# Kernel tuning notes

Measured on AMD Instinct MI355X. Metric: run time of the kernel, lower is better.

The kernel has to match this reference:

```python
import jax, jax.numpy as jnp
import numpy as np

B, T, H = 512, 128, 512
ZS, ZT = 128, 64
N_STATIC_CONT = 16
STATIC_CAT_KS = (8, 5, 12)
N_TEMP_CONT = 24
N_IRR = 2  # irreversible temp-cat indices 1 and 3; non-irr heads have widths 6,10,4
GRU_IN = ZT + H + 1 + N_IRR  # 579
TAU = 1.0


def _gumbel_softmax(logits, u, tau=TAU):
    # soft gumbel-softmax; u ~ Uniform(0,1), gumbel = -log(-log(u))
    g = -jnp.log(-jnp.log(u + 1e-10) + 1e-10)
    return jax.nn.softmax((logits + g) / tau, axis=-1)


def _gru_cell(x, h, Wih, Whh, bih, bhh):
    # PyTorch GRU cell semantics (gates in r,z,n order)
    gi = x @ Wih + bih
    gh = h @ Whh + bhh
    ir, iz, inn = jnp.split(gi, 3, axis=-1)
    hr, hz, hn = jnp.split(gh, 3, axis=-1)
    r = jax.nn.sigmoid(ir + hr)
    z = jax.nn.sigmoid(iz + hz)
    n = jnp.tanh(inn + r * hn)
    return (1.0 - z) * n + z * h


def setup_inputs():
    key = jax.random.key(0)
    ks = iter(jax.random.split(key, 64))
    def nrm(shape, fan_in):
        return jax.random.normal(next(ks), shape, jnp.float32) / np.sqrt(fan_in).astype(np.float32)
    def unif(shape):
        return jax.random.uniform(next(ks), shape, jnp.float32, 1e-6, 1.0 - 1e-6)
    return {
        "z_static": jax.random.normal(next(ks), (B, ZS), jnp.float32),
        "z_temporal": jax.random.normal(next(ks), (B, T, ZT), jnp.float32),
        "lengths": jax.random.randint(next(ks), (B,), 1, T + 1),
        "Ws1": nrm((ZS, H), ZS), "bs1": jnp.zeros((H,), jnp.float32),
        "Ws2": nrm((H, H), H), "bs2": jnp.zeros((H,), jnp.float32),
        "W_sc": nrm((H, N_STATIC_CONT), H), "b_sc": jnp.zeros((N_STATIC_CONT,), jnp.float32),
        "W_cat0": nrm((H, 8), H), "b_cat0": jnp.zeros((8,), jnp.float32),
        "W_cat1": nrm((H, 5), H), "b_cat1": jnp.zeros((5,), jnp.float32),
        "W_cat2": nrm((H, 12), H), "b_cat2": jnp.zeros((12,), jnp.float32),
        "W_irr": nrm((N_IRR, H, 2), H), "b_irr": jnp.zeros((N_IRR, 2), jnp.float32),
        "Wih0": nrm((GRU_IN, 3 * H), GRU_IN), "Whh0": nrm((H, 3 * H), H),
        "bih0": jnp.zeros((3 * H,), jnp.float32), "bhh0": jnp.zeros((3 * H,), jnp.float32),
        "Wih1": nrm((H, 3 * H), H), "Whh1": nrm((H, 3 * H), H),
        "bih1": jnp.zeros((3 * H,), jnp.float32), "bhh1": jnp.zeros((3 * H,), jnp.float32),
        "W_tc": nrm((H, N_TEMP_CONT), H), "b_tc": jnp.zeros((N_TEMP_CONT,), jnp.float32),
        "W_tcat0": nrm((H, 6), H), "b_tcat0": jnp.zeros((6,), jnp.float32),
        "W_tcat2": nrm((H, 10), H), "b_tcat2": jnp.zeros((10,), jnp.float32),
        "W_tcat4": nrm((H, 4), H), "b_tcat4": jnp.zeros((4,), jnp.float32),
        "W_hz": nrm((N_IRR, H + 1), H + 1), "b_hz": jnp.zeros((N_IRR,), jnp.float32),
        "u_sc0": unif((B, 8)), "u_sc1": unif((B, 5)), "u_sc2": unif((B, 12)),
        "u_irr": unif((N_IRR, B, 2)),
        "u_t0": unif((T, B, 6)), "u_t2": unif((T, B, 10)), "u_t4": unif((T, B, 4)),
        "u_bern": unif((T, B, N_IRR)),
    }


def reference(z_static, z_temporal, lengths, Ws1, bs1, Ws2, bs2, W_sc, b_sc,
              W_cat0, b_cat0, W_cat1, b_cat1, W_cat2, b_cat2, W_irr, b_irr,
              Wih0, Whh0, bih0, bhh0, Wih1, Whh1, bih1, bhh1,
              W_tc, b_tc, W_tcat0, b_tcat0, W_tcat2, b_tcat2, W_tcat4, b_tcat4,
              W_hz, b_hz, u_sc0, u_sc1, u_sc2, u_irr, u_t0, u_t2, u_t4, u_bern):
    baseline = jax.nn.relu(jax.nn.relu(z_static @ Ws1 + bs1) @ Ws2 + bs2)  # [B,H]
    static_cont = jax.nn.sigmoid(baseline @ W_sc + b_sc)
    static_cat = jnp.concatenate([
        _gumbel_softmax(baseline @ W_cat0 + b_cat0, u_sc0),
        _gumbel_softmax(baseline @ W_cat1 + b_cat1, u_sc1),
        _gumbel_softmax(baseline @ W_cat2 + b_cat2, u_sc2)], axis=-1)
    # init irreversible states = P(class 1) of 2-way gumbel-softmax per head
    irr0 = jnp.stack([
        _gumbel_softmax(baseline @ W_irr[j] + b_irr[j], u_irr[j])[:, 1]
        for j in range(N_IRR)], axis=-1)  # [B, N_IRR]
    tgrid = jnp.linspace(0.0, 1.0, T)
    visit_mask = (jnp.arange(T)[None, :] < lengths[:, None]).astype(jnp.float32)[..., None]  # [B,T,1]

    def step(carry, xs):
        h, irr = carry
        zt, ts, g0, g2, g4, ub = xs
        ts_col = jnp.broadcast_to(ts.reshape(1, 1), (zt.shape[0], 1))
        x = jnp.concatenate([zt, baseline, ts_col, irr], axis=-1)  # [B, GRU_IN]
        h0 = _gru_cell(x, h[0], Wih0, Whh0, bih0, bhh0)
        h1 = _gru_cell(h0, h[1], Wih1, Whh1, bih1, bhh1)
        out = h1
        tc = jax.nn.sigmoid(out @ W_tc + b_tc)
        # hazard heads take [out, t]; bernoulli flip only where not yet flipped
        haz = jax.nn.sigmoid(jnp.concatenate([out, ts_col], axis=-1) @ W_hz.T + b_hz)  # [B,N_IRR]
        flip = (ub < haz * (1.0 - irr)).astype(jnp.float32)
        irr_new = jnp.minimum(irr + flip, 1.0)
        tcat = jnp.concatenate([
            _gumbel_softmax(out @ W_tcat0 + b_tcat0, g0),
            irr_new[:, 0:1],
            _gumbel_softmax(out @ W_tcat2 + b_tcat2, g2),
            irr_new[:, 1:2],
            _gumbel_softmax(out @ W_tcat4 + b_tcat4, g4)], axis=-1)  # [B,22]
        return (jnp.stack([h0, h1]), irr_new), (tc, tcat)

    h_init = jnp.zeros((2, B, H), jnp.float32)
    _, (tc_seq, tcat_seq) = jax.lax.scan(
        step, (h_init, irr0),
        (jnp.swapaxes(z_temporal, 0, 1), tgrid, u_t0, u_t2, u_t4, u_bern))
    temporal_cont = jnp.swapaxes(tc_seq, 0, 1) * visit_mask  # [B,T,24]
    temporal_cat = jnp.swapaxes(tcat_seq, 0, 1) * visit_mask  # [B,T,22]
    visit_times = jnp.broadcast_to(tgrid[None, :], (B, T))
    return (static_cont, static_cat, temporal_cont, temporal_cat, visit_mask, visit_times)
```

## Files before the change

kernel.cpp:

```cpp
#include <hip/hip_runtime.h>


#define OFF_HID    0u
#define OFF_BASE   262144u
#define OFF_WHH0P  524288u
#define OFF_WIH1P  1310720u
#define OFF_WHH1P  2097152u
#define OFF_WMIDP  2883584u
#define OFF_WTOPP  3670016u
#define OFF_WTS    3768320u
#define OFF_WIRR   3769856u
#define OFF_GI0S   3772928u
#define OFF_H0X    4559360u
#define OFF_H1X    4821504u
#define OFF_HWTC   5083648u
#define OFF_HWHZ   5095936u
#define OFF_HWT0   5097088u
#define OFF_HWT2   5100160u
#define OFF_HWT4   5105280u
#define OFF_IRR0   5107328u
#define OFF_CTR    5108352u
#define OFF_END    5108864u

#define OUT_SC   0u
#define OUT_SCAT 8192u
#define OUT_TC   20992u
#define OUT_TCAT 1593856u
#define OUT_VM   3035648u
#define OUT_VT   3101184u

#define AS 516
#define RS 97

__device__ __forceinline__ float sigm(float x) { return 1.0f / (1.0f + expf(-x)); }
__device__ __forceinline__ float gumb(float u) { return -logf(-logf(u + 1e-10f) + 1e-10f); }
__device__ __forceinline__ float dot4(float4 a, float4 b) {
  return fmaf(a.x, b.x, fmaf(a.y, b.y, fmaf(a.z, b.z, a.w * b.w)));
}
__device__ __forceinline__ void astore(float* p, float v) {
  __hip_atomic_store(p, v, __ATOMIC_RELAXED, __HIP_MEMORY_SCOPE_AGENT);
}

__global__ __launch_bounds__(256) void pack_kernel(
    const float* __restrict__ Wih0, const float* __restrict__ Whh0,
    const float* __restrict__ Wih1, const float* __restrict__ Whh1,
    const float* __restrict__ W_tc, const float* __restrict__ W_hz,
    const float* __restrict__ W_tcat0, const float* __restrict__ W_tcat2,
    const float* __restrict__ W_tcat4, float* __restrict__ ws) {
  int idx = blockIdx.x * 256 + threadIdx.x;
  if (idx < 3145728) {
    int m = idx / 786432, r = idx % 786432;
    int s = r / 49152, t = r % 49152;
    if (m < 3) {
      int k4 = t / 384, rem = t % 384;
      int j = rem >> 7, u = (rem >> 2) & 31, ki = rem & 3;
      int k = 4 * k4 + ki;
      int col = j * 512 + s * 32 + u;
      const float* M = (m == 0) ? Whh0 : (m == 1) ? Wih1 : Whh1;
      unsigned dst = (m == 0) ? OFF_WHH0P : (m == 1) ? OFF_WIH1P : OFF_WHH1P;
      ws[dst + (unsigned)r] = M[k * 1536 + col];
    } else {
      int c = t / 512, k = t % 512;
      int col = (c % 3) * 512 + s * 32 + c / 3;
      ws[OFF_WMIDP + (unsigned)r] = Wih0[(64 + k) * 1536 + col];
    }
    return;
  }
  idx -= 3145728;
  if (idx < 98304) {
    int s = idx / 6144, t = idx % 6144;
    int k4 = t / 384, rem = t % 384;
    int j = rem >> 7, u = (rem >> 2) & 31, ki = rem & 3;
    int k = 4 * k4 + ki;
    int col = j * 512 + s * 32 + u;
    ws[OFF_WTOPP + (unsigned)idx] = Wih0[k * 1536 + col];
    return;
  }
  idx -= 98304;
  if (idx < 1536) {
    int s = idx / 96, c = idx % 96;
    ws[OFF_WTS + (unsigned)idx] = Wih0[576 * 1536 + (c % 3) * 512 + s * 32 + (c / 3)];
    return;
  }
  idx -= 1536;
  if (idx < 3072) {
    int s = idx / 192, m = (idx % 192) / 96, c = idx % 96;
    ws[OFF_WIRR + (unsigned)idx] = Wih0[(577 + m) * 1536 + (c % 3) * 512 + s * 32 + (c / 3)];
    return;
  }
  idx -= 3072;
  if (idx < 12288) { int c = idx / 512, k = idx % 512; ws[OFF_HWTC + (unsigned)idx] = W_tc[k * 24 + c]; return; }
  idx -= 12288;
  if (idx < 1032) {
    int c = idx / 516, j = idx % 516;
    ws[OFF_HWHZ + (unsigned)idx] = (j < 513) ? W_hz[c * 513 + j] : 0.0f;
    return;
  }
  idx -= 1032;
  if (idx < 3072) { int c = idx / 512, k = idx % 512; ws[OFF_HWT0 + (unsigned)idx] = W_tcat0[k * 6 + c]; return; }
  idx -= 3072;
  if (idx < 5120) { int c = idx / 512, k = idx % 512; ws[OFF_HWT2 + (unsigned)idx] = W_tcat2[k * 10 + c]; return; }
  idx -= 5120;
  if (idx < 2048) { int c = idx / 512, k = idx % 512; ws[OFF_HWT4 + (unsigned)idx] = W_tcat4[k * 4 + c]; }
}

template <int K>
__global__ __launch_bounds__(256) void mlp_kernel(
    const float* __restrict__ X, const float* __restrict__ Wm,
    const float* __restrict__ bias, float* __restrict__ Y) {
  __shared__ float Xs[4][K];
  const int rt = blockIdx.x, tid = threadIdx.x;
  for (int i = tid; i < 4 * K; i += 256) Xs[i / K][i % K] = X[(rt * 4 + i / K) * K + (i % K)];
  __syncthreads();
  float acc[4][2] = {};
  const int c0 = tid, c1 = tid + 256;
  for (int k = 0; k < K; ++k) {
    float w0 = Wm[k * 512 + c0], w1 = Wm[k * 512 + c1];
#pragma unroll
    for (int r = 0; r < 4; ++r) {
      acc[r][0] = fmaf(Xs[r][k], w0, acc[r][0]);
      acc[r][1] = fmaf(Xs[r][k], w1, acc[r][1]);
    }
  }
#pragma unroll
  for (int r = 0; r < 4; ++r) {
    Y[(rt * 4 + r) * 512 + c0] = fmaxf(acc[r][0] + bias[c0], 0.0f);
    Y[(rt * 4 + r) * 512 + c1] = fmaxf(acc[r][1] + bias[c1], 0.0f);
  }
}

__global__ __launch_bounds__(256) void gi0_kernel(
    const float* __restrict__ baseline, const float* __restrict__ WmidP,
    const float* __restrict__ bih0, float* __restrict__ gi0s) {
  __shared__ float As[64][128];
  __shared__ float Bs[96][129];
  const int s = blockIdx.x >> 3, rt = blockIdx.x & 7;
  const int tid = threadIdx.x, cg = tid & 31, rg = tid >> 5;
  float acc[8][3] = {};
  for (int kc = 0; kc < 4; ++kc) {
    for (int i = tid; i < 2048; i += 256) {
      int r = i >> 5, k4 = (i & 31) << 2;
      *(float4*)&As[r][k4] = *(const float4*)&baseline[(rt * 64 + r) * 512 + kc * 128 + k4];
    }
    for (int i = tid; i < 3072; i += 256) {
      int c = i >> 5, k4 = (i & 31) << 2;
      float4 v = *(const float4*)&WmidP[((unsigned)s * 96 + c) * 512 + kc * 128 + k4];
      Bs[c][k4] = v.x; Bs[c][k4 + 1] = v.y; Bs[c][k4 + 2] = v.z; Bs[c][k4 + 3] = v.w;
    }
    __syncthreads();
    for (int kk = 0; kk < 128; ++kk) {
      float b0 = Bs[3 * cg + 0][kk], b1 = Bs[3 * cg + 1][kk], b2 = Bs[3 * cg + 2][kk];
#pragma unroll
      for (int r = 0; r < 8; ++r) {
        float a = As[rg * 8 + r][kk];
        acc[r][0] = fmaf(a, b0, acc[r][0]);
        acc[r][1] = fmaf(a, b1, acc[r][1]);
        acc[r][2] = fmaf(a, b2, acc[r][2]);
      }
    }
    __syncthreads();
  }
#pragma unroll
  for (int r = 0; r < 8; ++r)
#pragma unroll
    for (int j = 0; j < 3; ++j) {
      int c = 3 * cg + j;
      gi0s[((unsigned)s * 512 + rt * 64 + rg * 8 + r) * 96 + c] = acc[r][j] + bih0[j * 512 + s * 32 + cg];
    }
}

__device__ void gumbel_write(const float* logits, int w, const float* u, float* dst) {
  float e[12]; float mx = -1e30f;
#pragma unroll
  for (int i = 0; i < 12; ++i) if (i < w) { e[i] = logits[i] + gumb(u[i]); mx = fmaxf(mx, e[i]); }
  float sum = 0.0f;
#pragma unroll
  for (int i = 0; i < 12; ++i) if (i < w) { e[i] = expf(e[i] - mx); sum += e[i]; }
  float inv = 1.0f / sum;
#pragma unroll
  for (int i = 0; i < 12; ++i) if (i < w) dst[i] = e[i] * inv;
}

__global__ __launch_bounds__(64) void static_heads_kernel(
    const float* __restrict__ baseline,
    const float* __restrict__ W_sc, const float* __restrict__ b_sc,
    const float* __restrict__ W_cat0, const float* __restrict__ b_cat0,
    const float* __restrict__ W_cat1, const float* __restrict__ b_cat1,
    const float* __restrict__ W_cat2, const float* __restrict__ b_cat2,
    const float* __restrict__ W_irr, const float* __restrict__ b_irr,
    const float* __restrict__ u_sc0, const float* __restrict__ u_sc1,
    const float* __restrict__ u_sc2, const float* __restrict__ u_irr,
    float* __restrict__ out, float* __restrict__ irr0buf) {
  const int b = blockIdx.x, tid = threadIdx.x;
  __shared__ float br[512];
  __shared__ float dots[48];
  for (int i = tid; i < 512; i += 64) br[i] = baseline[b * 512 + i];
  __syncthreads();
  if (tid < 45) {
    float d = 0.0f;
    if (tid < 16) { for (int k = 0; k < 512; ++k) d = fmaf(br[k], W_sc[k * 16 + tid], d); d += b_sc[tid]; }
    else if (tid < 24) { int c = tid - 16; for (int k = 0; k < 512; ++k) d = fmaf(br[k], W_cat0[k * 8 + c], d); d += b_cat0[c]; }
    else if (tid < 29) { int c = tid - 24; for (int k = 0; k < 512; ++k) d = fmaf(br[k], W_cat1[k * 5 + c], d); d += b_cat1[c]; }
    else if (tid < 41) { int c = tid - 29; for (int k = 0; k < 512; ++k) d = fmaf(br[k], W_cat2[k * 12 + c], d); d += b_cat2[c]; }
    else { int i = tid - 41, j = i >> 1, cls = i & 1;
           for (int k = 0; k < 512; ++k) d = fmaf(br[k], W_irr[j * 1024 + k * 2 + cls], d);
           d += b_irr[j * 2 + cls]; }
    dots[tid] = d;
  }
  __syncthreads();
  if (tid < 16) out[OUT_SC + b * 16 + tid] = sigm(dots[tid]);
  else if (tid == 16) gumbel_write(&dots[16], 8,  u_sc0 + b * 8,  out + OUT_SCAT + b * 25 + 0);
  else if (tid == 17) gumbel_write(&dots[24], 5,  u_sc1 + b * 5,  out + OUT_SCAT + b * 25 + 8);
  else if (tid == 18) gumbel_write(&dots[29], 12, u_sc2 + b * 12, out + OUT_SCAT + b * 25 + 13);
  else if (tid == 19 || tid == 20) {
    int j = tid - 19;
    float e0 = dots[41 + 2 * j] + gumb(u_irr[j * 1024 + b * 2 + 0]);
    float e1 = dots[42 + 2 * j] + gumb(u_irr[j * 1024 + b * 2 + 1]);
    float mx = fmaxf(e0, e1);
    float x0 = expf(e0 - mx), x1 = expf(e1 - mx);
    irr0buf[b * 2 + j] = x1 / (x0 + x1);
  }
}

__global__ __launch_bounds__(1024, 4) void recurrence_kernel(
    float* ws, const float* __restrict__ z_temporal, const int* __restrict__ lengths,
    const float* __restrict__ bhh0, const float* __restrict__ bih1, const float* __restrict__ bhh1,
    const float* __restrict__ b_tc, const float* __restrict__ b_hz,
    const float* __restrict__ b_tcat0, const float* __restrict__ b_tcat2,
    const float* __restrict__ b_tcat4,
    const float* __restrict__ u_t0, const float* __restrict__ u_t2,
    const float* __restrict__ u_t4, const float* __restrict__ u_bern,
    float* __restrict__ out) {
  const int tid = threadIdx.x;
  const int s = blockIdx.x & 15;
  const int g = blockIdx.x >> 4;
  const int b0 = g * 32;
  const int lane = tid & 63, wv = tid >> 6;
  const int kh = wv >> 3;
  const int cq = (wv >> 1) & 3;
  const int rh = wv & 1;
  const int u8 = lane & 7;
  const int rg8 = lane >> 3;
  const int unit = 8 * cq + u8;
  const int jglob = s * 32 + unit;
  const int row0 = 16 * rh + rg8;
  const int hrow = tid >> 5, kp = tid & 31;

  __shared__ __align__(16) float A0[32 * AS];
  __shared__ __align__(16) float A1[32 * AS];
  __shared__ __align__(16) float Rbuf[2 * 32 * RS];
  __shared__ float irr_l[32][2];

  float* h0x = ws + OFF_H0X;
  float* h1x = ws + OFF_H1X;
  unsigned* ctr = ((unsigned*)(ws + OFF_CTR)) + g * 32;

  const float* WpA = ws + OFF_WHH0P + (unsigned)s * 49152;
  const float* WpI = ws + OFF_WIH1P + (unsigned)s * 49152;
  const float* WpH = ws + OFF_WHH1P + (unsigned)s * 49152;
  const float* WpT = ws + OFF_WTOPP + (unsigned)s * 6144;

  const int c0u = 3 * unit;
  const float* wtsp  = ws + OFF_WTS + s * 96;
  const float* wirrp = ws + OFF_WIRR + s * 192;
  const float* gi0p  = ws + OFF_GI0S + ((unsigned)s * 512 + b0) * 96;
  float wts0 = wtsp[c0u], wts1 = wtsp[c0u + 1], wts2 = wtsp[c0u + 2];
  float wi00 = wirrp[c0u], wi01 = wirrp[c0u + 1], wi02 = wirrp[c0u + 2];
  float wi10 = wirrp[96 + c0u], wi11 = wirrp[96 + c0u + 1], wi12 = wirrp[96 + c0u + 2];
  float g0s[2][3];
#pragma unroll
  for (int q = 0; q < 2; ++q)
#pragma unroll
    for (int j = 0; j < 3; ++j) g0s[q][j] = gi0p[(row0 + 8 * q) * 96 + c0u + j];
  float bh0r = bhh0[jglob], bh0z = bhh0[512 + jglob], bh0n = bhh0[1024 + jglob];
  float bi1r = bih1[jglob], bi1z = bih1[512 + jglob], bi1n = bih1[1024 + jglob];
  float bh1r = bhh1[jglob], bh1z = bhh1[512 + jglob], bh1n = bhh1[1024 + jglob];
  float bhz0 = b_hz[0], bhz1 = b_hz[1];

  for (int i = tid; i < 32 * AS; i += 1024) { A0[i] = 0.0f; A1[i] = 0.0f; }
  if (tid < 64) irr_l[tid >> 1][tid & 1] = ws[OFF_IRR0 + (b0 + (tid >> 1)) * 2 + (tid & 1)];
  __syncthreads();

  unsigned bart = 0;
  auto barrive = [&]() {
    __builtin_amdgcn_s_waitcnt(0);
    __syncthreads();
    bart += 16;
    if (tid == 0)
      __hip_atomic_fetch_add(ctr, 1u, __ATOMIC_RELEASE, __HIP_MEMORY_SCOPE_AGENT);
  };
  auto barwait = [&]() {
    if (tid == 0) {
      while (__hip_atomic_load(ctr, __ATOMIC_RELAXED, __HIP_MEMORY_SCOPE_AGENT) < bart)
        __builtin_amdgcn_s_sleep(1);
    }
    __syncthreads();
    __asm__ __volatile__("" ::: "memory");
  };

  float4 sv[4];
  auto stage_issue = [&](const float* src) {
#pragma unroll
    for (int j = 0; j < 4; ++j) {
      int slot = j * 1024 + tid;
      asm volatile("global_load_dwordx4 %0, %1, off sc1"
                   : "=v"(sv[j]) : "v"(src + (slot >> 7) * 512 + ((slot & 127) << 2)));
    }
  };
  auto stage_finish = [&](float* dstLDS) {
    asm volatile("s_waitcnt vmcnt(0)" ::: "memory");
#pragma unroll
    for (int j = 0; j < 4; ++j) {
      int slot = j * 1024 + tid;
      *(float4*)(dstLDS + (slot >> 7) * AS + ((slot & 127) << 2)) = sv[j];
    }
    __syncthreads();
  };

  auto gemmKS = [&](const float* A, const float* Bp, float (&acc)[2][3]) {
    const float* bp = Bp + (unsigned)(kh * 64) * 384 + (unsigned)unit * 4;
    const float* ap = A + (unsigned)row0 * AS + kh * 256;
#pragma unroll 4
    for (int k4 = 0; k4 < 64; ++k4) {
      const float* p = bp + (unsigned)k4 * 384;
      float4 w0 = *(const float4*)(p);
      float4 w1 = *(const float4*)(p + 128);
      float4 w2 = *(const float4*)(p + 256);
      float4 av[2];
#pragma unroll
      for (int q = 0; q < 2; ++q) av[q] = *(const float4*)(ap + q * (8 * AS) + k4 * 4);
      const float* w0a = (const float*)&w0;
      const float* w1a = (const float*)&w1;
      const float* w2a = (const float*)&w2;
#pragma unroll
      for (int q = 0; q < 2; ++q) {
        const float* aa = (const float*)&av[q];
#pragma unroll
        for (int i = 0; i < 4; ++i) {
          acc[q][0] = fmaf(aa[i], w0a[i], acc[q][0]);
          acc[q][1] = fmaf(aa[i], w1a[i], acc[q][1]);
          acc[q][2] = fmaf(aa[i], w2a[i], acc[q][2]);
        }
      }
    }
  };

  auto gemmZ = [&](int t, float (&acc)[2][3]) {
    const float* bp = WpT + (unsigned)(kh * 8) * 384 + (unsigned)unit * 4;
#pragma unroll 2
    for (int k4 = 0; k4 < 8; ++k4) {
      const float* p = bp + (unsigned)k4 * 384;
      float4 w0 = *(const float4*)(p);
      float4 w1 = *(const float4*)(p + 128);
      float4 w2 = *(const float4*)(p + 256);
      const float* w0a = (const float*)&w0;
      const float* w1a = (const float*)&w1;
      const float* w2a = (const float*)&w2;
#pragma unroll
      for (int q = 0; q < 2; ++q) {
        int row = b0 + row0 + 8 * q;
        float4 zv = *(const float4*)(z_temporal + ((unsigned)row * 128 + t) * 64 + kh * 32 + k4 * 4);
        const float* aa = (const float*)&zv;
#pragma unroll
        for (int i = 0; i < 4; ++i) {
          acc[q][0] = fmaf(aa[i], w0a[i], acc[q][0]);
          acc[q][1] = fmaf(aa[i], w1a[i], acc[q][1]);
          acc[q][2] = fmaf(aa[i], w2a[i], acc[q][2]);
        }
      }
    }
  };

  auto reduce2 = [&](float (&aX)[2][3], float (&aY)[2][3]) {
    if (kh == 1) {
#pragma unroll
      for (int q = 0; q < 2; ++q) {
        int row = row0 + 8 * q;
        float* p0 = Rbuf + row * RS + c0u;
        float* p1 = Rbuf + 32 * RS + row * RS + c0u;
        p0[0] = aX[q][0]; p0[1] = aX[q][1]; p0[2] = aX[q][2];
        p1[0] = aY[q][0]; p1[1] = aY[q][1]; p1[2] = aY[q][2];
      }
    }
    __syncthreads();
    if (kh == 0) {
#pragma unroll
      for (int q = 0; q < 2; ++q) {
        int row = row0 + 8 * q;
        const float* p0 = Rbuf + row * RS + c0u;
        const float* p1 = Rbuf + 32 * RS + row * RS + c0u;
        aX[q][0] += p0[0]; aX[q][1] += p0[1]; aX[q][2] += p0[2];
        aY[q][0] += p1[0]; aY[q][1] += p1[1]; aY[q][2] += p1[2];
      }
    }
  };

  auto do_heads = [&](int tp) {
    const float tsp = (float)tp * (1.0f / 127.0f);
    const float* Ar = A1 + hrow * AS;
    {
      const float* hz = ws + OFF_HWHZ;
      float d0 = 0.0f, d1 = 0.0f;
#pragma unroll
      for (int i = 0; i < 4; ++i) {
        int k = kp * 4 + 128 * i;
        float4 x = *(const float4*)(Ar + k);
        d0 += dot4(x, *(const float4*)(hz + k));
        d1 += dot4(x, *(const float4*)(hz + 516 + k));
      }
#pragma unroll
      for (int off = 1; off < 32; off <<= 1) { d0 += __shfl_xor(d0, off, 32); d1 += __shfl_xor(d1, off, 32); }
      if (kp == 0) {
        float h0v = sigm(d0 + tsp * hz[512] + bhz0);
        float h1v = sigm(d1 + tsp * hz[516 + 512] + bhz1);
        float i0 = irr_l[hrow][0], i1 = irr_l[hrow][1];
        const float* ub = u_bern + ((unsigned)tp * 512 + b0 + hrow) * 2;
        irr_l[hrow][0] = fminf(i0 + ((ub[0] < h0v * (1.0f - i0)) ? 1.0f : 0.0f), 1.0f);
        irr_l[hrow][1] = fminf(i1 + ((ub[1] < h1v * (1.0f - i1)) ? 1.0f : 0.0f), 1.0f);
      }
    }
    if (s < 12) {
      const float* wt = ws + OFF_HWTC + (unsigned)(2 * s) * 512;
      float d0 = 0.0f, d1 = 0.0f;
#pragma unroll
      for (int i = 0; i < 4; ++i) {
        int k = kp * 4 + 128 * i;
        float4 x = *(const float4*)(Ar + k);
        d0 += dot4(x, *(const float4*)(wt + k));
        d1 += dot4(x, *(const float4*)(wt + 512 + k));
      }
#pragma unroll
      for (int off = 1; off < 32; off <<= 1) { d0 += __shfl_xor(d0, off, 32); d1 += __shfl_xor(d1, off, 32); }
      if (kp == 0) {
        int brow = b0 + hrow;
        float msk = (tp < lengths[brow]) ? 1.0f : 0.0f;
        float* o = out + OUT_TC + ((unsigned)brow * 128 + tp) * 24 + 2 * s;
        o[0] = sigm(d0 + b_tc[2 * s]) * msk;
        o[1] = sigm(d1 + b_tc[2 * s + 1]) * msk;
      }
    } else if (s == 15) {
      if (kp == 0) {
        int brow = b0 + hrow;
        float msk = (tp < lengths[brow]) ? 1.0f : 0.0f;
        out[OUT_TCAT + ((unsigned)brow * 128 + tp) * 22 + 6]  = irr_l[hrow][0] * msk;
        out[OUT_TCAT + ((unsigned)brow * 128 + tp) * 22 + 17] = irr_l[hrow][1] * msk;
        out[OUT_VM + (unsigned)brow * 128 + tp] = msk;
        out[OUT_VT + (unsigned)brow * 128 + tp] = tsp;
      }
    } else {
      const int w = (s == 12) ? 6 : (s == 13) ? 10 : 4;
      const float* WT = ws + ((s == 12) ? OFF_HWT0 : (s == 13) ? OFF_HWT2 : OFF_HWT4);
      const float* bt = (s == 12) ? b_tcat0 : (s == 13) ? b_tcat2 : b_tcat4;
      const float* ut = (s == 12) ? u_t0 : (s == 13) ? u_t2 : u_t4;
      const int cbase = (s == 12) ? 0 : (s == 13) ? 7 : 18;
      float lg[10];
#pragma unroll
      for (int c = 0; c < 10; ++c) lg[c] = 0.0f;
#pragma unroll
      for (int i = 0; i < 4; ++i) {
        int k = kp * 4 + 128 * i;
        float4 x = *(const float4*)(Ar + k);
        for (int c = 0; c < w; ++c)
          lg[c] += dot4(x, *(const float4*)(WT + (unsigned)c * 512 + k));
      }
      for (int c = 0; c < w; ++c) {
#pragma unroll
        for (int off = 1; off < 32; off <<= 1) lg[c] += __shfl_xor(lg[c], off, 32);
      }
      if (kp == 0) {
        int brow = b0 + hrow;
        float msk = (tp < lengths[brow]) ? 1.0f : 0.0f;
        float e[10], mx = -1e30f;
        for (int c = 0; c < w; ++c) {
          float uu = ut[((unsigned)tp * 512 + brow) * (unsigned)w + c];
          e[c] = lg[c] + bt[c] + gumb(uu); mx = fmaxf(mx, e[c]);
        }
        float sum = 0.0f;
        for (int c = 0; c < w; ++c) { e[c] = expf(e[c] - mx); sum += e[c]; }
        float inv = 1.0f / sum;
        float* o = out + OUT_TCAT + ((unsigned)brow * 128 + tp) * 22 + cbase;
        for (int c = 0; c < w; ++c) o[c] = e[c] * inv * msk;
      }
    }
    __syncthreads();
  };

  float accH[2][3] = {};
  for (int t = 0; t < 128; ++t) {
    const float tsv = (float)t * (1.0f / 127.0f);

    float accI[2][3] = {};
    gemmZ(t, accI);

    if (t > 0) {
      stage_finish(A1);
      do_heads(t - 1);
    }

    reduce2(accH, accI);
    if (kh == 0) {
#pragma unroll
      for (int q = 0; q < 2; ++q) {
        int row = row0 + 8 * q;
        float i0 = irr_l[row][0], i1 = irr_l[row][1];
        float gir = accI[q][0] + g0s[q][0] + tsv * wts0 + i0 * wi00 + i1 * wi10;
        float giz = accI[q][1] + g0s[q][1] + tsv * wts1 + i0 * wi01 + i1 * wi11;
        float gin = accI[q][2] + g0s[q][2] + tsv * wts2 + i0 * wi02 + i1 * wi12;
        float rr = sigm(gir + accH[q][0] + bh0r);
        float zz = sigm(giz + accH[q][1] + bh0z);
        float nn = tanhf(gin + rr * (accH[q][2] + bh0n));
        float hp = A0[row * AS + jglob];
        astore(h0x + (unsigned)(b0 + row) * 512 + jglob, (1.0f - zz) * nn + zz * hp);
      }
    }

    barrive();
    float accH2[2][3] = {};
    gemmKS(A1, WpH, accH2);
    barwait();

    stage_issue(h0x + b0 * 512);
    stage_finish(A0);

    float accI2[2][3] = {};
    gemmKS(A0, WpI, accI2);
    reduce2(accH2, accI2);
    if (kh == 0) {
#pragma unroll
      for (int q = 0; q < 2; ++q) {
        int row = row0 + 8 * q;
        float rr = sigm(accI2[q][0] + bi1r + accH2[q][0] + bh1r);
        float zz = sigm(accI2[q][1] + bi1z + accH2[q][1] + bh1z);
        float nn = tanhf(accI2[q][2] + bi1n + rr * (accH2[q][2] + bh1n));
        float hp = A1[row * AS + jglob];
        astore(h1x + (unsigned)(b0 + row) * 512 + jglob, (1.0f - zz) * nn + zz * hp);
      }
    }

    barrive();
#pragma unroll
    for (int q = 0; q < 2; ++q) { accH[q][0] = accH[q][1] = accH[q][2] = 0.0f; }
    gemmKS(A0, WpA, accH);
    barwait();

    stage_issue(h1x + b0 * 512);
  }
  stage_finish(A1);
  do_heads(127);
}

extern "C" void kernel_launch(void* const* d_in, const int* in_sizes, int n_in,
                              void* d_out, int out_size, void* d_ws, size_t ws_size,
                              hipStream_t stream) {
  const float* z_static   = (const float*)d_in[0];
  const float* z_temporal = (const float*)d_in[1];
  const int*   lengths    = (const int*)d_in[2];
  const float* Ws1 = (const float*)d_in[3];
  const float* bs1 = (const float*)d_in[4];
  const float* Ws2 = (const float*)d_in[5];
  const float* bs2 = (const float*)d_in[6];
  const float* W_sc = (const float*)d_in[7];
  const float* b_sc = (const float*)d_in[8];
  const float* W_cat0 = (const float*)d_in[9];
  const float* b_cat0 = (const float*)d_in[10];
  const float* W_cat1 = (const float*)d_in[11];
  const float* b_cat1 = (const float*)d_in[12];
  const float* W_cat2 = (const float*)d_in[13];
  const float* b_cat2 = (const float*)d_in[14];
  const float* W_irr = (const float*)d_in[15];
  const float* b_irr = (const float*)d_in[16];
  const float* Wih0 = (const float*)d_in[17];
  const float* Whh0 = (const float*)d_in[18];
  const float* bih0 = (const float*)d_in[19];
  const float* bhh0 = (const float*)d_in[20];
  const float* Wih1 = (const float*)d_in[21];
  const float* Whh1 = (const float*)d_in[22];
  const float* bih1 = (const float*)d_in[23];
  const float* bhh1 = (const float*)d_in[24];
  const float* W_tc = (const float*)d_in[25];
  const float* b_tc = (const float*)d_in[26];
  const float* W_tcat0 = (const float*)d_in[27];
  const float* b_tcat0 = (const float*)d_in[28];
  const float* W_tcat2 = (const float*)d_in[29];
  const float* b_tcat2 = (const float*)d_in[30];
  const float* W_tcat4 = (const float*)d_in[31];
  const float* b_tcat4 = (const float*)d_in[32];
  const float* W_hz = (const float*)d_in[33];
  const float* b_hz = (const float*)d_in[34];
  const float* u_sc0 = (const float*)d_in[35];
  const float* u_sc1 = (const float*)d_in[36];
  const float* u_sc2 = (const float*)d_in[37];
  const float* u_irr = (const float*)d_in[38];
  const float* u_t0 = (const float*)d_in[39];
  const float* u_t2 = (const float*)d_in[40];
  const float* u_t4 = (const float*)d_in[41];
  const float* u_bern = (const float*)d_in[42];

  float* ws = (float*)d_ws;
  float* out = (float*)d_out;

  hipMemsetAsync((void*)(ws + OFF_CTR), 0, (size_t)(OFF_END - OFF_CTR) * sizeof(float), stream);

  pack_kernel<<<12783, 256, 0, stream>>>(Wih0, Whh0, Wih1, Whh1,
      W_tc, W_hz, W_tcat0, W_tcat2, W_tcat4, ws);
  mlp_kernel<128><<<128, 256, 0, stream>>>(z_static, Ws1, bs1, ws + OFF_HID);
  mlp_kernel<512><<<128, 256, 0, stream>>>(ws + OFF_HID, Ws2, bs2, ws + OFF_BASE);
  static_heads_kernel<<<512, 64, 0, stream>>>(ws + OFF_BASE, W_sc, b_sc,
      W_cat0, b_cat0, W_cat1, b_cat1, W_cat2, b_cat2, W_irr, b_irr,
      u_sc0, u_sc1, u_sc2, u_irr, out, ws + OFF_IRR0);
  gi0_kernel<<<128, 256, 0, stream>>>(ws + OFF_BASE, ws + OFF_WMIDP, bih0, ws + OFF_GI0S);
  recurrence_kernel<<<256, 1024, 0, stream>>>(ws, z_temporal, lengths,
      bhh0, bih1, bhh1, b_tc, b_hz, b_tcat0, b_tcat2, b_tcat4,
      u_t0, u_t2, u_t4, u_bern, out);
}
```

Before: 13.75 ms.

## Fuse Wih1 and Whh0 GEMMs over shared A0 with 4-way K-split register tiles

Interleaves the Wih1 and next-step Whh0 weight panels so a single pass over the freshly staged layer-0 hidden state computes both layer-1 input gates and the next layer-0 recurrent gates. The tiling changes from a 2-way K split with 2 rows x 1 unit per thread to a 4-way K split with 2 rows x 2 units per thread, reduced through shared memory in two stages. The z_temporal projection for the next step is moved into the barrier wait window, and the cell constants and biases are packed into one float4-readable table. The aim is fewer passes over A0, more register reuse per load, and hidden latency in the cross-block barrier, at the cost of extra __syncthreads in the reduction and higher register pressure.

```diff
diff --git a/kernel.cpp b/kernel.cpp
--- a/kernel.cpp
+++ b/kernel.cpp
@@ -3,24 +3,22 @@
 
 #define OFF_HID    0u
 #define OFF_BASE   262144u
-#define OFF_WHH0P  524288u
-#define OFF_WIH1P  1310720u
+#define OFF_WFUSE  524288u
 #define OFF_WHH1P  2097152u
 #define OFF_WMIDP  2883584u
 #define OFF_WTOPP  3670016u
-#define OFF_WTS    3768320u
-#define OFF_WIRR   3769856u
-#define OFF_GI0S   3772928u
-#define OFF_H0X    4559360u
-#define OFF_H1X    4821504u
-#define OFF_HWTC   5083648u
-#define OFF_HWHZ   5095936u
-#define OFF_HWT0   5097088u
-#define OFF_HWT2   5100160u
-#define OFF_HWT4   5105280u
-#define OFF_IRR0   5107328u
-#define OFF_CTR    5108352u
-#define OFF_END    5108864u
+#define OFF_CELLC  3768320u
+#define OFF_GI0S   3778560u
+#define OFF_H0X    4827136u
+#define OFF_H1X    5089280u
+#define OFF_HWTC   5351424u
+#define OFF_HWHZ   5363712u
+#define OFF_HWT0   5364752u
+#define OFF_HWT2   5367824u
+#define OFF_HWT4   5372944u
+#define OFF_IRR0   5374992u
+#define OFF_CTR    5376016u
+#define OFF_END    5376528u
 
 #define OUT_SC   0u
 #define OUT_SCAT 8192u
@@ -44,51 +42,72 @@
 __global__ __launch_bounds__(256) void pack_kernel(
     const float* __restrict__ Wih0, const float* __restrict__ Whh0,
     const float* __restrict__ Wih1, const float* __restrict__ Whh1,
+    const float* __restrict__ bhh0, const float* __restrict__ bih1,
+    const float* __restrict__ bhh1,
     const float* __restrict__ W_tc, const float* __restrict__ W_hz,
     const float* __restrict__ W_tcat0, const float* __restrict__ W_tcat2,
     const float* __restrict__ W_tcat4, float* __restrict__ ws) {
   int idx = blockIdx.x * 256 + threadIdx.x;
-  if (idx < 3145728) {
-    int m = idx / 786432, r = idx % 786432;
-    int s = r / 49152, t = r % 49152;
-    if (m < 3) {
-      int k4 = t / 384, rem = t % 384;
-      int j = rem >> 7, u = (rem >> 2) & 31, ki = rem & 3;
-      int k = 4 * k4 + ki;
-      int col = j * 512 + s * 32 + u;
-      const float* M = (m == 0) ? Whh0 : (m == 1) ? Wih1 : Whh1;
-      unsigned dst = (m == 0) ? OFF_WHH0P : (m == 1) ? OFF_WIH1P : OFF_WHH1P;
-      ws[dst + (unsigned)r] = M[k * 1536 + col];
-    } else {
-      int c = t / 512, k = t % 512;
-      int col = (c % 3) * 512 + s * 32 + c / 3;
-      ws[OFF_WMIDP + (unsigned)r] = Wih0[(64 + k) * 1536 + col];
-    }
+  if (idx < 1572864) {
+    int s = idx / 98304, t = idx % 98304;
+    int k2 = t / 384, rem = t % 384;
+    int panel = rem / 192, rem2 = rem % 192;
+    int gate = rem2 / 64, rem3 = rem2 % 64;
+    int pr = rem3 >> 2, q = rem3 & 3;
+    int pair = q >> 1, ki = q & 1;
+    int k = 2 * k2 + ki;
+    int col = gate * 512 + s * 32 + pair * 16 + pr;
+    ws[OFF_WFUSE + (unsigned)idx] = panel ? Whh0[k * 1536 + col] : Wih1[k * 1536 + col];
     return;
   }
-  idx -= 3145728;
+  idx -= 1572864;
+  if (idx < 786432) {
+    int s = idx / 49152, t = idx % 49152;
+    int k4 = t / 384, rem = t % 384;
+    int gate = rem / 128, rem2 = rem % 128;
+    int pair = rem2 / 64, rem3 = rem2 % 64;
+    int pr = rem3 >> 2, ki = rem3 & 3;
+    int k = 4 * k4 + ki;
+    int col = gate * 512 + s * 32 + pair * 16 + pr;
+    ws[OFF_WHH1P + (unsigned)idx] = Whh1[k * 1536 + col];
+    return;
+  }
+  idx -= 786432;
+  if (idx < 786432) {
+    int s = idx / 49152, t = idx % 49152;
+    int c = t / 512, k = t % 512;
+    int col = (c % 3) * 512 + s * 32 + c / 3;
+    ws[OFF_WMIDP + (unsigned)idx] = Wih0[(64 + k) * 1536 + col];
+    return;
+  }
+  idx -= 786432;
   if (idx < 98304) {
     int s = idx / 6144, t = idx % 6144;
     int k4 = t / 384, rem = t % 384;
-    int j = rem >> 7, u = (rem >> 2) & 31, ki = rem & 3;
+    int gate = rem / 128, rem2 = rem % 128;
+    int pair = rem2 / 64, rem3 = rem2 % 64;
+    int pr = rem3 >> 2, ki = rem3 & 3;
     int k = 4 * k4 + ki;
-    int col = j * 512 + s * 32 + u;
+    int col = gate * 512 + s * 32 + pair * 16 + pr;
     ws[OFF_WTOPP + (unsigned)idx] = Wih0[k * 1536 + col];
     return;
   }
   idx -= 98304;
-  if (idx < 1536) {
-    int s = idx / 96, c = idx % 96;
-    ws[OFF_WTS + (unsigned)idx] = Wih0[576 * 1536 + (c % 3) * 512 + s * 32 + (c / 3)];
+  if (idx < 10240) {
+    int s = idx / 640, rem = idx % 640;
+    int unit = rem / 20, q = rem % 20;
+    int base = s * 32 + unit;
+    float v = 0.0f;
+    if (q < 3)       v = Wih0[576 * 1536 + q * 512 + base];
+    else if (q < 6)  v = Wih0[577 * 1536 + (q - 3) * 512 + base];
+    else if (q < 9)  v = Wih0[578 * 1536 + (q - 6) * 512 + base];
+    else if (q < 12) v = bhh0[(q - 9) * 512 + base];
+    else if (q < 15) v = bih1[(q - 12) * 512 + base];
+    else if (q < 18) v = bhh1[(q - 15) * 512 + base];
+    ws[OFF_CELLC + (unsigned)idx] = v;
     return;
   }
-  idx -= 1536;
-  if (idx < 3072) {
-    int s = idx / 192, m = (idx % 192) / 96, c = idx % 96;
-    ws[OFF_WIRR + (unsigned)idx] = Wih0[(577 + m) * 1536 + (c % 3) * 512 + s * 32 + (c / 3)];
-    return;
-  }
-  idx -= 3072;
+  idx -= 10240;
   if (idx < 12288) { int c = idx / 512, k = idx % 512; ws[OFF_HWTC + (unsigned)idx] = W_tc[k * 24 + c]; return; }
   idx -= 12288;
   if (idx < 1032) {
@@ -164,8 +183,8 @@
   for (int r = 0; r < 8; ++r)
 #pragma unroll
     for (int j = 0; j < 3; ++j) {
-      int c = 3 * cg + j;
-      gi0s[((unsigned)s * 512 + rt * 64 + rg * 8 + r) * 96 + c] = acc[r][j] + bih0[j * 512 + s * 32 + cg];
+      gi0s[(((unsigned)s * 512 + rt * 64 + rg * 8 + r) * 32 + cg) * 4 + j] =
+          acc[r][j] + bih0[j * 512 + s * 32 + cg];
     }
 }
 
@@ -224,7 +243,6 @@
 
 __global__ __launch_bounds__(1024, 4) void recurrence_kernel(
     float* ws, const float* __restrict__ z_temporal, const int* __restrict__ lengths,
-    const float* __restrict__ bhh0, const float* __restrict__ bih1, const float* __restrict__ bhh1,
     const float* __restrict__ b_tc, const float* __restrict__ b_hz,
     const float* __restrict__ b_tcat0, const float* __restrict__ b_tcat2,
     const float* __restrict__ b_tcat4,
@@ -236,14 +254,11 @@
   const int g = blockIdx.x >> 4;
   const int b0 = g * 32;
   const int lane = tid & 63, wv = tid >> 6;
-  const int kh = wv >> 3;
-  const int cq = (wv >> 1) & 3;
-  const int rh = wv & 1;
-  const int u8 = lane & 7;
-  const int rg8 = lane >> 3;
-  const int unit = 8 * cq + u8;
-  const int jglob = s * 32 + unit;
-  const int row0 = 16 * rh + rg8;
+  const int kh = wv >> 2;
+  const int rv = wv & 3;
+  const int pr = lane & 15;
+  const int rs = lane >> 4;
+  const int r0 = rv * 8 + rs * 2;
   const int hrow = tid >> 5, kp = tid & 31;
 
   __shared__ __align__(16) float A0[32 * AS];
@@ -255,26 +270,11 @@
   float* h1x = ws + OFF_H1X;
   unsigned* ctr = ((unsigned*)(ws + OFF_CTR)) + g * 32;
 
-  const float* WpA = ws + OFF_WHH0P + (unsigned)s * 49152;
-  const float* WpI = ws + OFF_WIH1P + (unsigned)s * 49152;
+  const float* WpF = ws + OFF_WFUSE + (unsigned)s * 98304;
   const float* WpH = ws + OFF_WHH1P + (unsigned)s * 49152;
   const float* WpT = ws + OFF_WTOPP + (unsigned)s * 6144;
-
-  const int c0u = 3 * unit;
-  const float* wtsp  = ws + OFF_WTS + s * 96;
-  const float* wirrp = ws + OFF_WIRR + s * 192;
-  const float* gi0p  = ws + OFF_GI0S + ((unsigned)s * 512 + b0) * 96;
-  float wts0 = wtsp[c0u], wts1 = wtsp[c0u + 1], wts2 = wtsp[c0u + 2];
-  float wi00 = wirrp[c0u], wi01 = wirrp[c0u + 1], wi02 = wirrp[c0u + 2];
-  float wi10 = wirrp[96 + c0u], wi11 = wirrp[96 + c0u + 1], wi12 = wirrp[96 + c0u + 2];
-  float g0s[2][3];
-#pragma unroll
-  for (int q = 0; q < 2; ++q)
-#pragma unroll
-    for (int j = 0; j < 3; ++j) g0s[q][j] = gi0p[(row0 + 8 * q) * 96 + c0u + j];
-  float bh0r = bhh0[jglob], bh0z = bhh0[512 + jglob], bh0n = bhh0[1024 + jglob];
-  float bi1r = bih1[jglob], bi1z = bih1[512 + jglob], bi1n = bih1[1024 + jglob];
-  float bh1r = bhh1[jglob], bh1z = bhh1[512 + jglob], bh1n = bhh1[1024 + jglob];
+  const float* cellc = ws + OFF_CELLC + (unsigned)s * 640;
+  const float* gi0p = ws + OFF_GI0S + ((unsigned)s * 512 + b0) * 128;
   float bhz0 = b_hz[0], bhz1 = b_hz[1];
 
   for (int i = tid; i < 32 * AS; i += 1024) { A0[i] = 0.0f; A1[i] = 0.0f; }
@@ -317,82 +317,133 @@
     __syncthreads();
   };
 
-  auto gemmKS = [&](const float* A, const float* Bp, float (&acc)[2][3]) {
-    const float* bp = Bp + (unsigned)(kh * 64) * 384 + (unsigned)unit * 4;
-    const float* ap = A + (unsigned)row0 * AS + kh * 256;
+  auto gemmP = [&](const float* A, const float* Bp, float (&acc)[2][2][3]) {
+    const float* bp = Bp + (unsigned)kh * 12288 + pr * 4;
+    const float* ap = A + (unsigned)r0 * AS + kh * 128;
 #pragma unroll 4
-    for (int k4 = 0; k4 < 64; ++k4) {
+    for (int k4 = 0; k4 < 32; ++k4) {
       const float* p = bp + (unsigned)k4 * 384;
-      float4 w0 = *(const float4*)(p);
-      float4 w1 = *(const float4*)(p + 128);
-      float4 w2 = *(const float4*)(p + 256);
-      float4 av[2];
-#pragma unroll
-      for (int q = 0; q < 2; ++q) av[q] = *(const float4*)(ap + q * (8 * AS) + k4 * 4);
-      const float* w0a = (const float*)&w0;
-      const float* w1a = (const float*)&w1;
-      const float* w2a = (const float*)&w2;
-#pragma unroll
-      for (int q = 0; q < 2; ++q) {
-        const float* aa = (const float*)&av[q];
-#pragma unroll
-        for (int i = 0; i < 4; ++i) {
-          acc[q][0] = fmaf(aa[i], w0a[i], acc[q][0]);
-          acc[q][1] = fmaf(aa[i], w1a[i], acc[q][1]);
-          acc[q][2] = fmaf(aa[i], w2a[i], acc[q][2]);
-        }
-      }
-    }
-  };
-
-  auto gemmZ = [&](int t, float (&acc)[2][3]) {
-    const float* bp = WpT + (unsigned)(kh * 8) * 384 + (unsigned)unit * 4;
+      float4 b[3][2];
+#pragma unroll
+      for (int gg = 0; gg < 3; ++gg) {
+        b[gg][0] = *(const float4*)(p + gg * 128);
+        b[gg][1] = *(const float4*)(p + gg * 128 + 64);
+      }
+      float4 a0 = *(const float4*)(ap + k4 * 4);
+      float4 a1 = *(const float4*)(ap + AS + k4 * 4);
+      const float* a0a = (const float*)&a0;
+      const float* a1a = (const float*)&a1;
+#pragma unroll
+      for (int i = 0; i < 4; ++i)
+#pragma unroll
+        for (int gg = 0; gg < 3; ++gg) {
+          const float* bb = (const float*)&b[gg][0];
+          const float* bc = (const float*)&b[gg][1];
+          acc[0][0][gg] = fmaf(a0a[i], bb[i], acc[0][0][gg]);
+          acc[0][1][gg] = fmaf(a1a[i], bb[i], acc[0][1][gg]);
+          acc[1][0][gg] = fmaf(a0a[i], bc[i], acc[1][0][gg]);
+          acc[1][1][gg] = fmaf(a1a[i], bc[i], acc[1][1][gg]);
+        }
+    }
+  };
+
+  auto gemmF = [&](const float* A, float (&aI)[2][2][3], float (&aH)[2][2][3]) {
+    const float* bp = WpF + (unsigned)kh * 24576 + pr * 4;
+    const float* ap = A + (unsigned)r0 * AS + kh * 128;
 #pragma unroll 2
-    for (int k4 = 0; k4 < 8; ++k4) {
+    for (int k4 = 0; k4 < 32; ++k4) {
+      float4 a0 = *(const float4*)(ap + k4 * 4);
+      float4 a1 = *(const float4*)(ap + AS + k4 * 4);
+      const float* a0a = (const float*)&a0;
+      const float* a1a = (const float*)&a1;
+#pragma unroll
+      for (int h = 0; h < 2; ++h) {
+        const float* p = bp + (unsigned)(k4 * 2 + h) * 384;
+        float4 bi[3], bh[3];
+#pragma unroll
+        for (int gg = 0; gg < 3; ++gg) {
+          bi[gg] = *(const float4*)(p + gg * 64);
+          bh[gg] = *(const float4*)(p + 192 + gg * 64);
+        }
+#pragma unroll
+        for (int ki = 0; ki < 2; ++ki) {
+          float av0 = a0a[2 * h + ki], av1 = a1a[2 * h + ki];
+#pragma unroll
+          for (int gg = 0; gg < 3; ++gg) {
+            const float* bia = (const float*)&bi[gg];
+            const float* bha = (const float*)&bh[gg];
+            aI[0][0][gg] = fmaf(av0, bia[ki], aI[0][0][gg]);
+            aI[0][1][gg] = fmaf(av1, bia[ki], aI[0][1][gg]);
+            aI[1][0][gg] = fmaf(av0, bia[2 + ki], aI[1][0][gg]);
+            aI[1][1][gg] = fmaf(av1, bia[2 + ki], aI[1][1][gg]);
+            aH[0][0][gg] = fmaf(av0, bha[ki], aH[0][0][gg]);
+            aH[0][1][gg] = fmaf(av1, bha[ki], aH[0][1][gg]);
+            aH[1][0][gg] = fmaf(av0, bha[2 + ki], aH[1][0][gg]);
+            aH[1][1][gg] = fmaf(av1, bha[2 + ki], aH[1][1][gg]);
+          }
+        }
+      }
+    }
+  };
+
+  auto gemmZ = [&](int t, float (&acc)[2][2][3]) {
+    const float* bp = WpT + (unsigned)kh * 1536 + pr * 4;
+#pragma unroll
+    for (int k4 = 0; k4 < 4; ++k4) {
       const float* p = bp + (unsigned)k4 * 384;
-      float4 w0 = *(const float4*)(p);
-      float4 w1 = *(const float4*)(p + 128);
-      float4 w2 = *(const float4*)(p + 256);
-      const float* w0a = (const float*)&w0;
-      const float* w1a = (const float*)&w1;
-      const float* w2a = (const float*)&w2;
-#pragma unroll
-      for (int q = 0; q < 2; ++q) {
-        int row = b0 + row0 + 8 * q;
-        float4 zv = *(const float4*)(z_temporal + ((unsigned)row * 128 + t) * 64 + kh * 32 + k4 * 4);
-        const float* aa = (const float*)&zv;
-#pragma unroll
-        for (int i = 0; i < 4; ++i) {
-          acc[q][0] = fmaf(aa[i], w0a[i], acc[q][0]);
-          acc[q][1] = fmaf(aa[i], w1a[i], acc[q][1]);
-          acc[q][2] = fmaf(aa[i], w2a[i], acc[q][2]);
-        }
-      }
-    }
-  };
-
-  auto reduce2 = [&](float (&aX)[2][3], float (&aY)[2][3]) {
-    if (kh == 1) {
-#pragma unroll
-      for (int q = 0; q < 2; ++q) {
-        int row = row0 + 8 * q;
-        float* p0 = Rbuf + row * RS + c0u;
-        float* p1 = Rbuf + 32 * RS + row * RS + c0u;
-        p0[0] = aX[q][0]; p0[1] = aX[q][1]; p0[2] = aX[q][2];
-        p1[0] = aY[q][0]; p1[1] = aY[q][1]; p1[2] = aY[q][2];
-      }
-    }
-    __syncthreads();
-    if (kh == 0) {
-#pragma unroll
-      for (int q = 0; q < 2; ++q) {
-        int row = row0 + 8 * q;
-        const float* p0 = Rbuf + row * RS + c0u;
-        const float* p1 = Rbuf + 32 * RS + row * RS + c0u;
-        aX[q][0] += p0[0]; aX[q][1] += p0[1]; aX[q][2] += p0[2];
-        aY[q][0] += p1[0]; aY[q][1] += p1[1]; aY[q][2] += p1[2];
-      }
-    }
+      float4 b[3][2];
+#pragma unroll
+      for (int gg = 0; gg < 3; ++gg) {
+        b[gg][0] = *(const float4*)(p + gg * 128);
+        b[gg][1] = *(const float4*)(p + gg * 128 + 64);
+      }
+      float4 a0 = *(const float4*)(z_temporal + ((unsigned)(b0 + r0) * 128 + t) * 64 + kh * 16 + k4 * 4);
+      float4 a1 = *(const float4*)(z_temporal + ((unsigned)(b0 + r0 + 1) * 128 + t) * 64 + kh * 16 + k4 * 4);
+      const float* a0a = (const float*)&a0;
+      const float* a1a = (const float*)&a1;
+#pragma unroll
+      for (int i = 0; i < 4; ++i)
+#pragma unroll
+        for (int gg = 0; gg < 3; ++gg) {
+          const float* bb = (const float*)&b[gg][0];
+          const float* bc = (const float*)&b[gg][1];
+          acc[0][0][gg] = fmaf(a0a[i], bb[i], acc[0][0][gg]);
+          acc[0][1][gg] = fmaf(a1a[i], bb[i], acc[0][1][gg]);
+          acc[1][0][gg] = fmaf(a0a[i], bc[i], acc[1][0][gg]);
+          acc[1][1][gg] = fmaf(a1a[i], bc[i], acc[1][1][gg]);
+        }
+    }
+  };
+
+  auto reduce4 = [&](float (&a)[2][2][3]) {
+    auto wr = [&](int slot) {
+#pragma unroll
+      for (int p = 0; p < 2; ++p)
+#pragma unroll
+        for (int r = 0; r < 2; ++r) {
+          float* q = Rbuf + slot * (32 * RS) + (r0 + r) * RS + 3 * (pr + 16 * p);
+          q[0] = a[p][r][0]; q[1] = a[p][r][1]; q[2] = a[p][r][2];
+        }
+    };
+    auto ad = [&](int slot) {
+#pragma unroll
+      for (int p = 0; p < 2; ++p)
+#pragma unroll
+        for (int r = 0; r < 2; ++r) {
+          const float* q = Rbuf + slot * (32 * RS) + (r0 + r) * RS + 3 * (pr + 16 * p);
+          a[p][r][0] += q[0]; a[p][r][1] += q[1]; a[p][r][2] += q[2];
+        }
+    };
+    __syncthreads();
+    if (kh == 1) wr(0);
+    if (kh == 3) wr(1);
+    __syncthreads();
+    if (kh == 0) ad(0);
+    if (kh == 2) ad(1);
+    __syncthreads();
+    if (kh == 2) wr(0);
+    __syncthreads();
+    if (kh == 0) ad(0);
   };
 
   auto do_heads = [&](int tp) {
@@ -485,62 +536,86 @@
     __syncthreads();
   };
 
-  float accH[2][3] = {};
+  float accH[2][2][3] = {};
+  float accZ[2][2][3] = {};
+  gemmZ(0, accZ);
+
   for (int t = 0; t < 128; ++t) {
     const float tsv = (float)t * (1.0f / 127.0f);
-
-    float accI[2][3] = {};
-    gemmZ(t, accI);
 
     if (t > 0) {
       stage_finish(A1);
       do_heads(t - 1);
     }
 
-    reduce2(accH, accI);
+    reduce4(accH);
+    reduce4(accZ);
+
     if (kh == 0) {
 #pragma unroll
-      for (int q = 0; q < 2; ++q) {
-        int row = row0 + 8 * q;
-        float i0 = irr_l[row][0], i1 = irr_l[row][1];
-        float gir = accI[q][0] + g0s[q][0] + tsv * wts0 + i0 * wi00 + i1 * wi10;
-        float giz = accI[q][1] + g0s[q][1] + tsv * wts1 + i0 * wi01 + i1 * wi11;
-        float gin = accI[q][2] + g0s[q][2] + tsv * wts2 + i0 * wi02 + i1 * wi12;
-        float rr = sigm(gir + accH[q][0] + bh0r);
-        float zz = sigm(giz + accH[q][1] + bh0z);
-        float nn = tanhf(gin + rr * (accH[q][2] + bh0n));
-        float hp = A0[row * AS + jglob];
-        astore(h0x + (unsigned)(b0 + row) * 512 + jglob, (1.0f - zz) * nn + zz * hp);
+      for (int p = 0; p < 2; ++p) {
+        int u = pr + 16 * p, jg = s * 32 + u;
+        float4 cw = *(const float4*)(cellc + u * 20);
+        float4 ci = *(const float4*)(cellc + u * 20 + 4);
+        float4 cb = *(const float4*)(cellc + u * 20 + 8);
+#pragma unroll
+        for (int r = 0; r < 2; ++r) {
+          int row = r0 + r;
+          float4 g0 = *(const float4*)(gi0p + ((unsigned)row * 32 + u) * 4);
+          float i0 = irr_l[row][0], i1 = irr_l[row][1];
+          float gir = accZ[p][r][0] + g0.x + tsv * cw.x + i0 * cw.w + i1 * ci.z;
+          float giz = accZ[p][r][1] + g0.y + tsv * cw.y + i0 * ci.x + i1 * ci.w;
+          float gin = accZ[p][r][2] + g0.z + tsv * cw.z + i0 * ci.y + i1 * cb.x;
+          float rr = sigm(gir + accH[p][r][0] + cb.y);
+          float zz = sigm(giz + accH[p][r][1] + cb.z);
+          float nn = tanhf(gin + rr * (accH[p][r][2] + cb.w));
+          float hp = A0[row * AS + jg];
+          astore(h0x + (unsigned)(b0 + row) * 512 + jg, (1.0f - zz) * nn + zz * hp);
+        }
       }
     }
 
     barrive();
-    float accH2[2][3] = {};
-    gemmKS(A1, WpH, accH2);
+    float accH2[2][2][3] = {};
+    gemmP(A1, WpH, accH2);
     barwait();
+    reduce4(accH2);
 
     stage_issue(h0x + b0 * 512);
     stage_finish(A0);
 
-    float accI2[2][3] = {};
-    gemmKS(A0, WpI, accI2);
-    reduce2(accH2, accI2);
+    float accI2[2][2][3] = {};
+#pragma unroll
+    for (int p = 0; p < 2; ++p)
+#pragma unroll
+      for (int r = 0; r < 2; ++r) { accH[p][r][0] = accH[p][r][1] = accH[p][r][2] = 0.0f; }
+    gemmF(A0, accI2, accH);
+    reduce4(accI2);
+
     if (kh == 0) {
 #pragma unroll
-      for (int q = 0; q < 2; ++q) {
-        int row = row0 + 8 * q;
-        float rr = sigm(accI2[q][0] + bi1r + accH2[q][0] + bh1r);
-        float zz = sigm(accI2[q][1] + bi1z + accH2[q][1] + bh1z);
-        float nn = tanhf(accI2[q][2] + bi1n + rr * (accH2[q][2] + bh1n));
-        float hp = A1[row * AS + jglob];
-        astore(h1x + (unsigned)(b0 + row) * 512 + jglob, (1.0f - zz) * nn + zz * hp);
+      for (int p = 0; p < 2; ++p) {
+        int u = pr + 16 * p, jg = s * 32 + u;
+        float4 cc = *(const float4*)(cellc + u * 20 + 12);
+        float4 cd = *(const float4*)(cellc + u * 20 + 16);
+#pragma unroll
+        for (int r = 0; r < 2; ++r) {
+          int row = r0 + r;
+          float rr = sigm(accI2[p][r][0] + cc.x + accH2[p][r][0] + cc.w);
+          float zz = sigm(accI2[p][r][1] + cc.y + accH2[p][r][1] + cd.x);
+          float nn = tanhf(accI2[p][r][2] + cc.z + rr * (accH2[p][r][2] + cd.y));
+          float hp = A1[row * AS + jg];
+          astore(h1x + (unsigned)(b0 + row) * 512 + jg, (1.0f - zz) * nn + zz * hp);
+        }
       }
     }
 
     barrive();
 #pragma unroll
-    for (int q = 0; q < 2; ++q) { accH[q][0] = accH[q][1] = accH[q][2] = 0.0f; }
-    gemmKS(A0, WpA, accH);
+    for (int p = 0; p < 2; ++p)
+#pragma unroll
+      for (int r = 0; r < 2; ++r) { accZ[p][r][0] = accZ[p][r][1] = accZ[p][r][2] = 0.0f; }
+    if (t < 127) gemmZ(t + 1, accZ);
     barwait();
 
     stage_issue(h1x + b0 * 512);
@@ -601,8 +676,8 @@
 
   hipMemsetAsync((void*)(ws + OFF_CTR), 0, (size_t)(OFF_END - OFF_CTR) * sizeof(float), stream);
 
-  pack_kernel<<<12783, 256, 0, stream>>>(Wih0, Whh0, Wih1, Whh1,
-      W_tc, W_hz, W_tcat0, W_tcat2, W_tcat4, ws);
+  pack_kernel<<<12805, 256, 0, stream>>>(Wih0, Whh0, Wih1, Whh1,
+      bhh0, bih1, bhh1, W_tc, W_hz, W_tcat0, W_tcat2, W_tcat4, ws);
   mlp_kernel<128><<<128, 256, 0, stream>>>(z_static, Ws1, bs1, ws + OFF_HID);
   mlp_kernel<512><<<128, 256, 0, stream>>>(ws + OFF_HID, Ws2, bs2, ws + OFF_BASE);
   static_heads_kernel<<<512, 64, 0, stream>>>(ws + OFF_BASE, W_sc, b_sc,
@@ -610,6 +685,6 @@
       u_sc0, u_sc1, u_sc2, u_irr, out, ws + OFF_IRR0);
   gi0_kernel<<<128, 256, 0, stream>>>(ws + OFF_BASE, ws + OFF_WMIDP, bih0, ws + OFF_GI0S);
   recurrence_kernel<<<256, 1024, 0, stream>>>(ws, z_temporal, lengths,
-      bhh0, bih1, bhh1, b_tc, b_hz, b_tcat0, b_tcat2, b_tcat4,
+      b_tc, b_hz, b_tcat0, b_tcat2, b_tcat4,
       u_t0, u_t2, u_t4, u_bern, out);
 }
```

Result: slower. 16.44 ms (+19.6%).
